# Kernel tuning notes

Hardware: AMD Instinct MI355X
Metric: run time of the kernel (lower is better)

Reference implementation:

```python
import jax, jax.numpy as jnp
import numpy as np

E = 1024   # embedding_dim
H = 16     # heads
W = 1024   # lag / seq length
B = 4      # batch
D = E // H # head dim


def setup_inputs() -> dict:
    key = jax.random.key(0)
    ks = jax.random.split(key, 5)
    scale = E ** -0.5
    return {
        "x":   jax.random.normal(ks[0], (3, B, E, W), dtype=jnp.float32),
        "L_Q": jax.random.normal(ks[1], (E, E), dtype=jnp.float32) * scale,
        "L_K": jax.random.normal(ks[2], (E, E), dtype=jnp.float32) * scale,
        "L_V": jax.random.normal(ks[3], (E, E), dtype=jnp.float32) * scale,
        "M":   jax.random.normal(ks[4], (E, E), dtype=jnp.float32) * (1.0 / (2 * E)) ** 0.5,
        "b":   jnp.zeros((E, 1), dtype=jnp.float32),
    }


def reference(x, L_Q, L_K, L_V, M, b):
    # x: [3, B, E, W] channels-first; x[0]=K input, x[1]=Q input, x[2]=V input
    K = jnp.einsum('ef,bfw->bew', L_K, x[0])
    Q = jnp.einsum('ef,bfw->bew', L_Q, x[1])
    V = jnp.einsum('ef,bfw->bew', L_V, x[2])
    # reshape to [B, H, D, W]
    Kv = K.reshape(B, H, D, W)
    Qv = Q.reshape(B, H, D, W)
    Vv = V.reshape(B, H, D, W)
    # scores[b,h,q,k] = Q_v^T @ K_v
    scores = jnp.einsum('bhdq,bhdk->bhqk', Qv, Kv)
    # causal mask: -inf for q > k (strictly lower triangle), added BEFORE softmax
    q_idx = jnp.arange(W)[:, None]
    k_idx = jnp.arange(W)[None, :]
    mask = jnp.where(q_idx > k_idx, -jnp.inf, 0.0).astype(scores.dtype)
    scores = scores + mask
    # NON-STANDARD: softmax over the QUERY axis (dim=-2), then scale
    attn = jax.nn.softmax(scores, axis=-2) / (E ** 0.5)
    # V_v @ scores: [B,H,D,W] @ [B,H,W,W] -> [B,H,D,W]
    out = jnp.einsum('bhdq,bhqk->bhdk', Vv, attn).reshape(B, E, W)
    # dense: M @ out + b (dropout identity at inference)
    return jnp.einsum('oe,bew->bow', M, out) + b
```

## Files before the change

### kernel.cpp

```cpp
#include <hip/hip_runtime.h>
#include <stdint.h>
#include <math.h>

#define E_DIM 1024
#define W_DIM 1024
#define EW 1048576L

typedef _Float16 h16;
typedef __attribute__((ext_vector_type(8))) _Float16 h8;
typedef __attribute__((ext_vector_type(4))) float f4;

__device__ __forceinline__ void async_copy16(h16* lds, const h16* g) {
    __builtin_amdgcn_global_load_lds(
        (const __attribute__((address_space(1))) void*)g,
        (__attribute__((address_space(3))) void*)lds, 16, 0, 0);
}

__global__ __launch_bounds__(256) void cvt_w(
    const float* __restrict__ a, const float* __restrict__ b,
    const float* __restrict__ c, const float* __restrict__ d,
    h16* __restrict__ out)
{
    const float* srcs[4] = {a, b, c, d};
    const int z = blockIdx.y;
    const int i = blockIdx.x * 256 + threadIdx.x;
    if (i < 262144) {
        float4 v = reinterpret_cast<const float4*>(srcs[z])[i];
        union { h16 h[4]; uint2 u; } o;
        o.h[0] = (h16)v.x; o.h[1] = (h16)v.y; o.h[2] = (h16)v.z; o.h[3] = (h16)v.w;
        reinterpret_cast<uint2*>(out + z * EW)[i] = o.u;
    }
}

__global__ __launch_bounds__(256) void cvt_t(
    const float* __restrict__ x, h16* __restrict__ xt)
{
    __shared__ float Ts[64][65];
    const long sb = blockIdx.z;
    const float* src = x + sb * EW;
    h16* dst = xt + sb * EW;
    const int e0 = blockIdx.y * 64, w0 = blockIdx.x * 64;
    const int r = threadIdx.x >> 4, c4 = (threadIdx.x & 15) * 4;

    #pragma unroll
    for (int p = 0; p < 4; ++p) {
        float4 v = *reinterpret_cast<const float4*>(src + (long)(e0 + r + p * 16) * W_DIM + w0 + c4);
        Ts[c4 + 0][r + p * 16] = v.x;
        Ts[c4 + 1][r + p * 16] = v.y;
        Ts[c4 + 2][r + p * 16] = v.z;
        Ts[c4 + 3][r + p * 16] = v.w;
    }
    __syncthreads();
    #pragma unroll
    for (int p = 0; p < 4; ++p) {
        int wr = r + p * 16;
        union { h16 h[4]; uint2 u; } o;
        o.h[0] = (h16)Ts[wr][c4 + 0];
        o.h[1] = (h16)Ts[wr][c4 + 1];
        o.h[2] = (h16)Ts[wr][c4 + 2];
        o.h[3] = (h16)Ts[wr][c4 + 3];
        *reinterpret_cast<uint2*>(dst + (long)(w0 + wr) * E_DIM + e0 + c4) = o.u;
    }
}

__global__ __launch_bounds__(256) void gemm_proj3(
    const h16* __restrict__ xh, const h16* __restrict__ Wts,
    h16* __restrict__ KQV)
{
    __shared__ h16 As[128 * 32];
    __shared__ h16 Bs[128 * 32];

    const int t = threadIdx.x;
    const int wave = t >> 6, lane = t & 63;
    const int quad = lane >> 4, l16 = lane & 15;
    const int m0 = blockIdx.y * 128, n0 = blockIdx.x * 128;
    const int wm = (wave >> 1) * 64, wn = (wave & 1) * 64;

    const int proj = blockIdx.z >> 2, bz = blockIdx.z & 3;
    const h16 *A, *Bt; h16* C;
    if (proj == 0)      { A = xh + bz * EW;       Bt = Wts;          C = KQV + bz * EW; }
    else if (proj == 1) { A = xh + (4 + bz) * EW; Bt = Wts + EW;     C = KQV + (4 + bz) * EW; }
    else                { A = Wts + 2 * EW;       Bt = xh + (8 + bz) * EW; C = KQV + (8 + bz) * EW; }

    const int sr = t >> 2;
    const int sg = (t & 3) * 8;

    f4 acc[4][4] = {};

    for (int k0 = 0; k0 < 1024; k0 += 32) {
        __syncthreads();
        async_copy16(As + sr * 32 + sg,        A  + (long)(m0 + sr) * E_DIM + k0 + sg);
        async_copy16(As + (sr + 64) * 32 + sg, A  + (long)(m0 + sr + 64) * E_DIM + k0 + sg);
        async_copy16(Bs + sr * 32 + sg,        Bt + (long)(n0 + sr) * E_DIM + k0 + sg);
        async_copy16(Bs + (sr + 64) * 32 + sg, Bt + (long)(n0 + sr + 64) * E_DIM + k0 + sg);
        __syncthreads();

        h8 av[4], bv[4];
        #pragma unroll
        for (int i = 0; i < 4; ++i) {
            av[i] = *reinterpret_cast<const h8*>(As + (wm + i * 16 + l16) * 32 + quad * 8);
            bv[i] = *reinterpret_cast<const h8*>(Bs + (wn + i * 16 + l16) * 32 + quad * 8);
        }
        #pragma unroll
        for (int mt = 0; mt < 4; ++mt)
            #pragma unroll
            for (int nt = 0; nt < 4; ++nt)
                acc[mt][nt] = __builtin_amdgcn_mfma_f32_16x16x32_f16(av[mt], bv[nt], acc[mt][nt], 0, 0, 0);
    }

    #pragma unroll
    for (int mt = 0; mt < 4; ++mt)
        #pragma unroll
        for (int i = 0; i < 4; ++i) {
            int m = m0 + wm + mt * 16 + quad * 4 + i;
            #pragma unroll
            for (int nt = 0; nt < 4; ++nt)
                C[(long)m * W_DIM + n0 + wn + nt * 16 + l16] = (h16)acc[mt][nt][i];
        }
}

__global__ __launch_bounds__(256) void gemm_out(
    const h16* __restrict__ A, const h16* __restrict__ Bt, long sBz,
    float* __restrict__ C, long sCz, const float* __restrict__ bias)
{
    __shared__ h16 As[128 * 40];
    __shared__ h16 Bs[128 * 40];

    const int t = threadIdx.x;
    const int wave = t >> 6, lane = t & 63;
    const int quad = lane >> 4, l16 = lane & 15;
    const int m0 = blockIdx.y * 128, n0 = blockIdx.x * 128;
    const int wm = (wave >> 1) * 64, wn = (wave & 1) * 64;
    Bt += blockIdx.z * sBz;

    const int sr = t >> 2;
    const int sg = (t & 3) * 8;

    f4 acc[4][4] = {};

    uint4 a0 = *reinterpret_cast<const uint4*>(A  + (long)(m0 + sr) * E_DIM + sg);
    uint4 a1 = *reinterpret_cast<const uint4*>(A  + (long)(m0 + sr + 64) * E_DIM + sg);
    uint4 b0 = *reinterpret_cast<const uint4*>(Bt + (long)(n0 + sr) * E_DIM + sg);
    uint4 b1 = *reinterpret_cast<const uint4*>(Bt + (long)(n0 + sr + 64) * E_DIM + sg);

    for (int k0 = 0; k0 < 1024; k0 += 32) {
        __syncthreads();
        *reinterpret_cast<uint4*>(As + sr * 40 + sg)        = a0;
        *reinterpret_cast<uint4*>(As + (sr + 64) * 40 + sg) = a1;
        *reinterpret_cast<uint4*>(Bs + sr * 40 + sg)        = b0;
        *reinterpret_cast<uint4*>(Bs + (sr + 64) * 40 + sg) = b1;
        __syncthreads();

        if (k0 + 32 < 1024) {
            a0 = *reinterpret_cast<const uint4*>(A  + (long)(m0 + sr) * E_DIM + k0 + 32 + sg);
            a1 = *reinterpret_cast<const uint4*>(A  + (long)(m0 + sr + 64) * E_DIM + k0 + 32 + sg);
            b0 = *reinterpret_cast<const uint4*>(Bt + (long)(n0 + sr) * E_DIM + k0 + 32 + sg);
            b1 = *reinterpret_cast<const uint4*>(Bt + (long)(n0 + sr + 64) * E_DIM + k0 + 32 + sg);
        }

        h8 av[4], bv[4];
        #pragma unroll
        for (int i = 0; i < 4; ++i) {
            av[i] = *reinterpret_cast<const h8*>(As + (wm + i * 16 + l16) * 40 + quad * 8);
            bv[i] = *reinterpret_cast<const h8*>(Bs + (wn + i * 16 + l16) * 40 + quad * 8);
        }
        #pragma unroll
        for (int mt = 0; mt < 4; ++mt)
            #pragma unroll
            for (int nt = 0; nt < 4; ++nt)
                acc[mt][nt] = __builtin_amdgcn_mfma_f32_16x16x32_f16(av[mt], bv[nt], acc[mt][nt], 0, 0, 0);
    }

    float* Cf = C + blockIdx.z * sCz;
    #pragma unroll
    for (int mt = 0; mt < 4; ++mt)
        #pragma unroll
        for (int i = 0; i < 4; ++i) {
            int m = m0 + wm + mt * 16 + quad * 4 + i;
            float bv_ = bias ? bias[m] : 0.f;
            #pragma unroll
            for (int nt = 0; nt < 4; ++nt)
                Cf[(long)m * W_DIM + n0 + wn + nt * 16 + l16] = acc[mt][nt][i] + bv_;
        }
}

__global__ __launch_bounds__(256) void attn_mfma(
    const h16* __restrict__ Kt, const h16* __restrict__ Qt,
    const h16* __restrict__ V, h16* __restrict__ AoT)
{
    __shared__ h16 Ks[64 * 72];
    __shared__ h16 Qs[64 * 72];
    __shared__ h16 Vs[64 * 72];
    __shared__ h16 Ps[4][16 * 72];

    const int t = threadIdx.x, wave = t >> 6, lane = t & 63;
    const int quad = lane >> 4, l16 = lane & 15;
    const int b = blockIdx.y >> 4, h = blockIdx.y & 15;
    const int k0 = blockIdx.x * 64;
    const int kw = wave * 16;

    const h16* Ktb = Kt + (long)b * EW + h * 64;
    const h16* Qtb = Qt + (long)b * EW + h * 64;
    const h16* Vb  = V  + (long)b * EW + (long)(h * 64) * W_DIM;

    const int sr = t >> 2;
    const int sg = (t & 3) * 8;

    uint4 ka = *reinterpret_cast<const uint4*>(Ktb + (long)(k0 + sr) * E_DIM + sg);
    uint4 kb = *reinterpret_cast<const uint4*>(Ktb + (long)(k0 + sr) * E_DIM + sg + 32);
    uint4 qa = *reinterpret_cast<const uint4*>(Qtb + (long)sr * E_DIM + sg);
    uint4 qb = *reinterpret_cast<const uint4*>(Qtb + (long)sr * E_DIM + sg + 32);
    uint4 va = *reinterpret_cast<const uint4*>(Vb + (long)sr * W_DIM + sg);
    uint4 vb = *reinterpret_cast<const uint4*>(Vb + (long)sr * W_DIM + sg + 32);

    float mrow[4], lrow[4];
    #pragma unroll
    for (int i = 0; i < 4; ++i) { mrow[i] = -1e30f; lrow[i] = 0.f; }
    f4 O[4] = {};

    for (int q0 = 0; q0 <= k0; q0 += 64) {
        __syncthreads();
        if (q0 == 0) {
            *reinterpret_cast<uint4*>(Ks + sr * 72 + sg)      = ka;
            *reinterpret_cast<uint4*>(Ks + sr * 72 + sg + 32) = kb;
        }
        *reinterpret_cast<uint4*>(Qs + sr * 72 + sg)      = qa;
        *reinterpret_cast<uint4*>(Qs + sr * 72 + sg + 32) = qb;
        *reinterpret_cast<uint4*>(Vs + sr * 72 + sg)      = va;
        *reinterpret_cast<uint4*>(Vs + sr * 72 + sg + 32) = vb;
        __syncthreads();

        if (q0 + 64 <= k0) {
            qa = *reinterpret_cast<const uint4*>(Qtb + (long)(q0 + 64 + sr) * E_DIM + sg);
            qb = *reinterpret_cast<const uint4*>(Qtb + (long)(q0 + 64 + sr) * E_DIM + sg + 32);
            va = *reinterpret_cast<const uint4*>(Vb + (long)sr * W_DIM + q0 + 64 + sg);
            vb = *reinterpret_cast<const uint4*>(Vb + (long)sr * W_DIM + q0 + 64 + sg + 32);
        }

        f4 S[4] = {};
        #pragma unroll
        for (int c = 0; c < 2; ++c) {
            h8 av = *reinterpret_cast<const h8*>(Ks + (kw + l16) * 72 + c * 32 + quad * 8);
            #pragma unroll
            for (int nt = 0; nt < 4; ++nt) {
                h8 bv = *reinterpret_cast<const h8*>(Qs + (nt * 16 + l16) * 72 + c * 32 + quad * 8);
                S[nt] = __builtin_amdgcn_mfma_f32_16x16x32_f16(av, bv, S[nt], 0, 0, 0);
            }
        }

        if (q0 == k0) {
            #pragma unroll
            for (int nt = 0; nt < 4; ++nt)
                #pragma unroll
                for (int i = 0; i < 4; ++i)
                    if (q0 + nt * 16 + l16 > k0 + kw + quad * 4 + i) S[nt][i] = -1e30f;
        }

        float al[4];
        #pragma unroll
        for (int i = 0; i < 4; ++i) {
            float mx = fmaxf(fmaxf(S[0][i], S[1][i]), fmaxf(S[2][i], S[3][i]));
            mx = fmaxf(mx, __shfl_xor(mx, 1));
            mx = fmaxf(mx, __shfl_xor(mx, 2));
            mx = fmaxf(mx, __shfl_xor(mx, 4));
            mx = fmaxf(mx, __shfl_xor(mx, 8));
            float nm = fmaxf(mrow[i], mx);
            al[i] = __expf(mrow[i] - nm);
            mrow[i] = nm;
        }
        #pragma unroll
        for (int nt = 0; nt < 4; ++nt)
            #pragma unroll
            for (int i = 0; i < 4; ++i)
                S[nt][i] = __expf(S[nt][i] - mrow[i]);
        #pragma unroll
        for (int i = 0; i < 4; ++i) {
            float sm = S[0][i] + S[1][i] + S[2][i] + S[3][i];
            sm += __shfl_xor(sm, 1);
            sm += __shfl_xor(sm, 2);
            sm += __shfl_xor(sm, 4);
            sm += __shfl_xor(sm, 8);
            lrow[i] = lrow[i] * al[i] + sm;
            #pragma unroll
            for (int dt = 0; dt < 4; ++dt) O[dt][i] *= al[i];
        }

        #pragma unroll
        for (int nt = 0; nt < 4; ++nt)
            #pragma unroll
            for (int i = 0; i < 4; ++i)
                Ps[wave][(quad * 4 + i) * 72 + nt * 16 + l16] = (h16)S[nt][i];
        asm volatile("" ::: "memory");

        #pragma unroll
        for (int c = 0; c < 2; ++c) {
            h8 pa = *reinterpret_cast<const h8*>(&Ps[wave][l16 * 72 + c * 32 + quad * 8]);
            #pragma unroll
            for (int dt = 0; dt < 4; ++dt) {
                h8 vv = *reinterpret_cast<const h8*>(Vs + (dt * 16 + l16) * 72 + c * 32 + quad * 8);
                O[dt] = __builtin_amdgcn_mfma_f32_16x16x32_f16(pa, vv, O[dt], 0, 0, 0);
            }
        }
    }

    #pragma unroll
    for (int dt = 0; dt < 4; ++dt)
        #pragma unroll
        for (int i = 0; i < 4; ++i)
            AoT[(long)b * EW + (long)(k0 + kw + quad * 4 + i) * E_DIM + h * 64 + dt * 16 + l16] =
                (h16)(O[dt][i] / lrow[i] * 0.03125f);
}

extern "C" void kernel_launch(void* const* d_in, const int* in_sizes, int n_in,
                              void* d_out, int out_size, void* d_ws, size_t ws_size,
                              hipStream_t stream)
{
    const float* x  = (const float*)d_in[0];
    const float* LQ = (const float*)d_in[1];
    const float* LK = (const float*)d_in[2];
    const float* LV = (const float*)d_in[3];
    const float* Mw = (const float*)d_in[4];
    const float* bb = (const float*)d_in[5];
    float* out = (float*)d_out;
    h16* ws = (h16*)d_ws;

    h16* xh  = ws;
    h16* LKh = ws + 12 * EW;
    h16* Mh  = ws + 15 * EW;
    h16* Kp  = ws + 16 * EW;
    h16* Qp  = ws + 20 * EW;
    h16* Vp  = ws + 24 * EW;
    h16* Ao  = ws + 28 * EW;

    cvt_w<<<dim3(1024, 4), 256, 0, stream>>>(LK, LQ, LV, Mw, LKh);
    cvt_t<<<dim3(16, 16, 12), 256, 0, stream>>>(x, xh);

    dim3 blk(256);
    gemm_proj3<<<dim3(8, 8, 12), blk, 0, stream>>>(xh, LKh, Kp);

    attn_mfma<<<dim3(16, 64), blk, 0, stream>>>(Kp, Qp, Vp, Ao);

    gemm_out<<<dim3(8, 8, 4), blk, 0, stream>>>(Mh, Ao, EW, out, EW, bb);
}
```

Measured before the change: 226.8 us.

## Fuse conversion kernels, async double-buffer attention and output GEMM, reorder tiles

Merges the weight conversion and input transpose into one prep launch. The attention kernel now keeps K fragments in registers, double-buffers Q/V tiles in XOR-swizzled LDS through async global-to-LDS copies, and launches the heaviest causal tiles first. The row-sum shuffle reduction is replaced by an MFMA against a ones vector. The output GEMM uses 64x128 tiles with async double-buffered LDS and folds the batch into the N dimension, adding more blocks at the cost of fewer accumulators per wave.

```diff
diff --git a/kernel.cpp b/kernel.cpp
--- a/kernel.cpp
+++ b/kernel.cpp
@@ -16,50 +16,51 @@
         (__attribute__((address_space(3))) void*)lds, 16, 0, 0);
 }
 
-__global__ __launch_bounds__(256) void cvt_w(
-    const float* __restrict__ a, const float* __restrict__ b,
-    const float* __restrict__ c, const float* __restrict__ d,
-    h16* __restrict__ out)
-{
-    const float* srcs[4] = {a, b, c, d};
-    const int z = blockIdx.y;
-    const int i = blockIdx.x * 256 + threadIdx.x;
-    if (i < 262144) {
-        float4 v = reinterpret_cast<const float4*>(srcs[z])[i];
-        union { h16 h[4]; uint2 u; } o;
-        o.h[0] = (h16)v.x; o.h[1] = (h16)v.y; o.h[2] = (h16)v.z; o.h[3] = (h16)v.w;
-        reinterpret_cast<uint2*>(out + z * EW)[i] = o.u;
-    }
-}
-
-__global__ __launch_bounds__(256) void cvt_t(
-    const float* __restrict__ x, h16* __restrict__ xt)
+__global__ __launch_bounds__(256) void prep(
+    const float* __restrict__ x, const float* __restrict__ LK,
+    const float* __restrict__ LQ, const float* __restrict__ LV,
+    const float* __restrict__ Mw, h16* __restrict__ xt, h16* __restrict__ wh)
 {
     __shared__ float Ts[64][65];
-    const long sb = blockIdx.z;
-    const float* src = x + sb * EW;
-    h16* dst = xt + sb * EW;
-    const int e0 = blockIdx.y * 64, w0 = blockIdx.x * 64;
-    const int r = threadIdx.x >> 4, c4 = (threadIdx.x & 15) * 4;
-
-    #pragma unroll
-    for (int p = 0; p < 4; ++p) {
-        float4 v = *reinterpret_cast<const float4*>(src + (long)(e0 + r + p * 16) * W_DIM + w0 + c4);
-        Ts[c4 + 0][r + p * 16] = v.x;
-        Ts[c4 + 1][r + p * 16] = v.y;
-        Ts[c4 + 2][r + p * 16] = v.z;
-        Ts[c4 + 3][r + p * 16] = v.w;
-    }
-    __syncthreads();
-    #pragma unroll
-    for (int p = 0; p < 4; ++p) {
-        int wr = r + p * 16;
-        union { h16 h[4]; uint2 u; } o;
-        o.h[0] = (h16)Ts[wr][c4 + 0];
-        o.h[1] = (h16)Ts[wr][c4 + 1];
-        o.h[2] = (h16)Ts[wr][c4 + 2];
-        o.h[3] = (h16)Ts[wr][c4 + 3];
-        *reinterpret_cast<uint2*>(dst + (long)(w0 + wr) * E_DIM + e0 + c4) = o.u;
+    const int z = blockIdx.z;
+    const int t = threadIdx.x;
+    if (z < 12) {
+        const float* src = x + (long)z * EW;
+        h16* dst = xt + (long)z * EW;
+        const int e0 = blockIdx.y * 64, w0 = blockIdx.x * 64;
+        const int r = t >> 4, c4 = (t & 15) * 4;
+        #pragma unroll
+        for (int p = 0; p < 4; ++p) {
+            float4 v = *reinterpret_cast<const float4*>(src + (long)(e0 + r + p * 16) * W_DIM + w0 + c4);
+            Ts[c4 + 0][r + p * 16] = v.x;
+            Ts[c4 + 1][r + p * 16] = v.y;
+            Ts[c4 + 2][r + p * 16] = v.z;
+            Ts[c4 + 3][r + p * 16] = v.w;
+        }
+        __syncthreads();
+        #pragma unroll
+        for (int p = 0; p < 4; ++p) {
+            int wr = r + p * 16;
+            union { h16 h[4]; uint2 u; } o;
+            o.h[0] = (h16)Ts[wr][c4 + 0];
+            o.h[1] = (h16)Ts[wr][c4 + 1];
+            o.h[2] = (h16)Ts[wr][c4 + 2];
+            o.h[3] = (h16)Ts[wr][c4 + 3];
+            *reinterpret_cast<uint2*>(dst + (long)(w0 + wr) * E_DIM + e0 + c4) = o.u;
+        }
+    } else {
+        const float* srcs[4] = {LK, LQ, LV, Mw};
+        const float* s = srcs[z - 12];
+        h16* o = wh + (long)(z - 12) * EW;
+        long base = ((long)(blockIdx.y * 16 + blockIdx.x)) * 1024 + t;
+        #pragma unroll
+        for (int k = 0; k < 4; ++k) {
+            long i = base + k * 256;
+            float4 v = reinterpret_cast<const float4*>(s)[i];
+            union { h16 h[4]; uint2 u; } u;
+            u.h[0] = (h16)v.x; u.h[1] = (h16)v.y; u.h[2] = (h16)v.z; u.h[3] = (h16)v.w;
+            reinterpret_cast<uint2*>(o)[i] = u.u;
+        }
     }
 }
 
@@ -120,67 +121,69 @@
 }
 
 __global__ __launch_bounds__(256) void gemm_out(
-    const h16* __restrict__ A, const h16* __restrict__ Bt, long sBz,
-    float* __restrict__ C, long sCz, const float* __restrict__ bias)
-{
-    __shared__ h16 As[128 * 40];
-    __shared__ h16 Bs[128 * 40];
+    const h16* __restrict__ A, const h16* __restrict__ Bt,
+    float* __restrict__ C, const float* __restrict__ bias)
+{
+    __shared__ h16 As[2][64 * 32];
+    __shared__ h16 Bs[2][128 * 32];
 
     const int t = threadIdx.x;
     const int wave = t >> 6, lane = t & 63;
     const int quad = lane >> 4, l16 = lane & 15;
-    const int m0 = blockIdx.y * 128, n0 = blockIdx.x * 128;
-    const int wm = (wave >> 1) * 64, wn = (wave & 1) * 64;
-    Bt += blockIdx.z * sBz;
-
-    const int sr = t >> 2;
-    const int sg = (t & 3) * 8;
-
-    f4 acc[4][4] = {};
-
-    uint4 a0 = *reinterpret_cast<const uint4*>(A  + (long)(m0 + sr) * E_DIM + sg);
-    uint4 a1 = *reinterpret_cast<const uint4*>(A  + (long)(m0 + sr + 64) * E_DIM + sg);
-    uint4 b0 = *reinterpret_cast<const uint4*>(Bt + (long)(n0 + sr) * E_DIM + sg);
-    uint4 b1 = *reinterpret_cast<const uint4*>(Bt + (long)(n0 + sr + 64) * E_DIM + sg);
-
-    for (int k0 = 0; k0 < 1024; k0 += 32) {
-        __syncthreads();
-        *reinterpret_cast<uint4*>(As + sr * 40 + sg)        = a0;
-        *reinterpret_cast<uint4*>(As + (sr + 64) * 40 + sg) = a1;
-        *reinterpret_cast<uint4*>(Bs + sr * 40 + sg)        = b0;
-        *reinterpret_cast<uint4*>(Bs + (sr + 64) * 40 + sg) = b1;
-        __syncthreads();
-
-        if (k0 + 32 < 1024) {
-            a0 = *reinterpret_cast<const uint4*>(A  + (long)(m0 + sr) * E_DIM + k0 + 32 + sg);
-            a1 = *reinterpret_cast<const uint4*>(A  + (long)(m0 + sr + 64) * E_DIM + k0 + 32 + sg);
-            b0 = *reinterpret_cast<const uint4*>(Bt + (long)(n0 + sr) * E_DIM + k0 + 32 + sg);
-            b1 = *reinterpret_cast<const uint4*>(Bt + (long)(n0 + sr + 64) * E_DIM + k0 + 32 + sg);
-        }
-
-        h8 av[4], bv[4];
-        #pragma unroll
-        for (int i = 0; i < 4; ++i) {
-            av[i] = *reinterpret_cast<const h8*>(As + (wm + i * 16 + l16) * 40 + quad * 8);
-            bv[i] = *reinterpret_cast<const h8*>(Bs + (wn + i * 16 + l16) * 40 + quad * 8);
-        }
-        #pragma unroll
-        for (int mt = 0; mt < 4; ++mt)
+    const int m0 = blockIdx.y * 64, n0 = blockIdx.x * 128;
+    const int wm = (wave >> 1) * 32, wn = (wave & 1) * 64;
+
+    f4 acc[2][4] = {};
+
+    const int ga_r = t >> 2, ga_c = (t & 3) * 8;
+
+    {
+        async_copy16(&As[0][t * 8], A + (long)(m0 + ga_r) * E_DIM + ga_c);
+        #pragma unroll
+        for (int j = 0; j < 2; ++j) {
+            int g = j * 256 + t;
+            async_copy16(&Bs[0][g * 8], Bt + (long)(n0 + (g >> 2)) * E_DIM + (g & 3) * 8);
+        }
+    }
+
+    for (int it = 0; it < 32; ++it) {
+        __syncthreads();
+        if (it + 1 < 32) {
+            int nb = (it + 1) & 1, k0 = (it + 1) * 32;
+            async_copy16(&As[nb][t * 8], A + (long)(m0 + ga_r) * E_DIM + k0 + ga_c);
+            #pragma unroll
+            for (int j = 0; j < 2; ++j) {
+                int g = j * 256 + t;
+                async_copy16(&Bs[nb][g * 8], Bt + (long)(n0 + (g >> 2)) * E_DIM + k0 + (g & 3) * 8);
+            }
+        }
+        const h16* as = As[it & 1];
+        const h16* bs = Bs[it & 1];
+        h8 av[2], bv[4];
+        #pragma unroll
+        for (int mt = 0; mt < 2; ++mt)
+            av[mt] = *reinterpret_cast<const h8*>(as + (wm + mt * 16 + l16) * 32 + quad * 8);
+        #pragma unroll
+        for (int nt = 0; nt < 4; ++nt)
+            bv[nt] = *reinterpret_cast<const h8*>(bs + (wn + nt * 16 + l16) * 32 + quad * 8);
+        #pragma unroll
+        for (int mt = 0; mt < 2; ++mt)
             #pragma unroll
             for (int nt = 0; nt < 4; ++nt)
                 acc[mt][nt] = __builtin_amdgcn_mfma_f32_16x16x32_f16(av[mt], bv[nt], acc[mt][nt], 0, 0, 0);
     }
 
-    float* Cf = C + blockIdx.z * sCz;
-    #pragma unroll
-    for (int mt = 0; mt < 4; ++mt)
+    #pragma unroll
+    for (int mt = 0; mt < 2; ++mt)
         #pragma unroll
         for (int i = 0; i < 4; ++i) {
             int m = m0 + wm + mt * 16 + quad * 4 + i;
             float bv_ = bias ? bias[m] : 0.f;
             #pragma unroll
-            for (int nt = 0; nt < 4; ++nt)
-                Cf[(long)m * W_DIM + n0 + wn + nt * 16 + l16] = acc[mt][nt][i] + bv_;
+            for (int nt = 0; nt < 4; ++nt) {
+                int n = n0 + wn + nt * 16 + l16;
+                C[(long)(n >> 10) * EW + (long)m * W_DIM + (n & 1023)] = acc[mt][nt][i] + bv_;
+            }
         }
 }
 
@@ -188,67 +191,69 @@
     const h16* __restrict__ Kt, const h16* __restrict__ Qt,
     const h16* __restrict__ V, h16* __restrict__ AoT)
 {
-    __shared__ h16 Ks[64 * 72];
-    __shared__ h16 Qs[64 * 72];
-    __shared__ h16 Vs[64 * 72];
+    __shared__ h16 Qs[2][64 * 64];
+    __shared__ h16 Vs[2][64 * 64];
     __shared__ h16 Ps[4][16 * 72];
 
     const int t = threadIdx.x, wave = t >> 6, lane = t & 63;
     const int quad = lane >> 4, l16 = lane & 15;
     const int b = blockIdx.y >> 4, h = blockIdx.y & 15;
-    const int k0 = blockIdx.x * 64;
+    const int kt = 15 - blockIdx.x;
+    const int k0 = kt * 64;
     const int kw = wave * 16;
 
     const h16* Ktb = Kt + (long)b * EW + h * 64;
     const h16* Qtb = Qt + (long)b * EW + h * 64;
     const h16* Vb  = V  + (long)b * EW + (long)(h * 64) * W_DIM;
 
-    const int sr = t >> 2;
-    const int sg = (t & 3) * 8;
-
-    uint4 ka = *reinterpret_cast<const uint4*>(Ktb + (long)(k0 + sr) * E_DIM + sg);
-    uint4 kb = *reinterpret_cast<const uint4*>(Ktb + (long)(k0 + sr) * E_DIM + sg + 32);
-    uint4 qa = *reinterpret_cast<const uint4*>(Qtb + (long)sr * E_DIM + sg);
-    uint4 qb = *reinterpret_cast<const uint4*>(Qtb + (long)sr * E_DIM + sg + 32);
-    uint4 va = *reinterpret_cast<const uint4*>(Vb + (long)sr * W_DIM + sg);
-    uint4 vb = *reinterpret_cast<const uint4*>(Vb + (long)sr * W_DIM + sg + 32);
-
-    float mrow[4], lrow[4];
-    #pragma unroll
-    for (int i = 0; i < 4; ++i) { mrow[i] = -1e30f; lrow[i] = 0.f; }
+    h8 av0 = *reinterpret_cast<const h8*>(Ktb + (long)(k0 + kw + l16) * E_DIM + quad * 8);
+    h8 av1 = *reinterpret_cast<const h8*>(Ktb + (long)(k0 + kw + l16) * E_DIM + 32 + quad * 8);
+
+    const int swz0 = ((quad) ^ (l16 & 7)) * 8;
+    const int swz1 = ((4 + quad) ^ (l16 & 7)) * 8;
+
+    float mrow[4], al[4];
+    #pragma unroll
+    for (int i = 0; i < 4; ++i) mrow[i] = -1e30f;
     f4 O[4] = {};
-
-    for (int q0 = 0; q0 <= k0; q0 += 64) {
-        __syncthreads();
-        if (q0 == 0) {
-            *reinterpret_cast<uint4*>(Ks + sr * 72 + sg)      = ka;
-            *reinterpret_cast<uint4*>(Ks + sr * 72 + sg + 32) = kb;
-        }
-        *reinterpret_cast<uint4*>(Qs + sr * 72 + sg)      = qa;
-        *reinterpret_cast<uint4*>(Qs + sr * 72 + sg + 32) = qb;
-        *reinterpret_cast<uint4*>(Vs + sr * 72 + sg)      = va;
-        *reinterpret_cast<uint4*>(Vs + sr * 72 + sg + 32) = vb;
-        __syncthreads();
-
-        if (q0 + 64 <= k0) {
-            qa = *reinterpret_cast<const uint4*>(Qtb + (long)(q0 + 64 + sr) * E_DIM + sg);
-            qb = *reinterpret_cast<const uint4*>(Qtb + (long)(q0 + 64 + sr) * E_DIM + sg + 32);
-            va = *reinterpret_cast<const uint4*>(Vb + (long)sr * W_DIM + q0 + 64 + sg);
-            vb = *reinterpret_cast<const uint4*>(Vb + (long)sr * W_DIM + q0 + 64 + sg + 32);
-        }
+    f4 Lacc = {};
+    h8 ones;
+    #pragma unroll
+    for (int j = 0; j < 8; ++j) ones[j] = (h16)1.0f;
+
+    #pragma unroll
+    for (int j = 0; j < 2; ++j) {
+        int g = j * 256 + t, row = g >> 3, cg = (g & 7) ^ (row & 7);
+        async_copy16(&Qs[0][g * 8], Qtb + (long)row * E_DIM + cg * 8);
+        async_copy16(&Vs[0][g * 8], Vb + (long)row * W_DIM + cg * 8);
+    }
+
+    for (int it = 0; it <= kt; ++it) {
+        const int q0 = it * 64;
+        __syncthreads();
+        if (it < kt) {
+            int nb = (it + 1) & 1, q1 = q0 + 64;
+            #pragma unroll
+            for (int j = 0; j < 2; ++j) {
+                int g = j * 256 + t, row = g >> 3, cg = (g & 7) ^ (row & 7);
+                async_copy16(&Qs[nb][g * 8], Qtb + (long)(q1 + row) * E_DIM + cg * 8);
+                async_copy16(&Vs[nb][g * 8], Vb + (long)row * W_DIM + q1 + cg * 8);
+            }
+        }
+        const h16* qs = Qs[it & 1];
+        const h16* vs = Vs[it & 1];
 
         f4 S[4] = {};
         #pragma unroll
-        for (int c = 0; c < 2; ++c) {
-            h8 av = *reinterpret_cast<const h8*>(Ks + (kw + l16) * 72 + c * 32 + quad * 8);
-            #pragma unroll
-            for (int nt = 0; nt < 4; ++nt) {
-                h8 bv = *reinterpret_cast<const h8*>(Qs + (nt * 16 + l16) * 72 + c * 32 + quad * 8);
-                S[nt] = __builtin_amdgcn_mfma_f32_16x16x32_f16(av, bv, S[nt], 0, 0, 0);
-            }
-        }
-
-        if (q0 == k0) {
+        for (int nt = 0; nt < 4; ++nt) {
+            int rb = (nt * 16 + l16) * 64;
+            h8 b0 = *reinterpret_cast<const h8*>(qs + rb + swz0);
+            h8 b1 = *reinterpret_cast<const h8*>(qs + rb + swz1);
+            S[nt] = __builtin_amdgcn_mfma_f32_16x16x32_f16(av0, b0, S[nt], 0, 0, 0);
+            S[nt] = __builtin_amdgcn_mfma_f32_16x16x32_f16(av1, b1, S[nt], 0, 0, 0);
+        }
+
+        if (it == kt) {
             #pragma unroll
             for (int nt = 0; nt < 4; ++nt)
                 #pragma unroll
@@ -256,7 +261,6 @@
                     if (q0 + nt * 16 + l16 > k0 + kw + quad * 4 + i) S[nt][i] = -1e30f;
         }
 
-        float al[4];
         #pragma unroll
         for (int i = 0; i < 4; ++i) {
             float mx = fmaxf(fmaxf(S[0][i], S[1][i]), fmaxf(S[2][i], S[3][i]));
@@ -275,12 +279,7 @@
                 S[nt][i] = __expf(S[nt][i] - mrow[i]);
         #pragma unroll
         for (int i = 0; i < 4; ++i) {
-            float sm = S[0][i] + S[1][i] + S[2][i] + S[3][i];
-            sm += __shfl_xor(sm, 1);
-            sm += __shfl_xor(sm, 2);
-            sm += __shfl_xor(sm, 4);
-            sm += __shfl_xor(sm, 8);
-            lrow[i] = lrow[i] * al[i] + sm;
+            Lacc[i] *= al[i];
             #pragma unroll
             for (int dt = 0; dt < 4; ++dt) O[dt][i] *= al[i];
         }
@@ -295,9 +294,11 @@
         #pragma unroll
         for (int c = 0; c < 2; ++c) {
             h8 pa = *reinterpret_cast<const h8*>(&Ps[wave][l16 * 72 + c * 32 + quad * 8]);
+            Lacc = __builtin_amdgcn_mfma_f32_16x16x32_f16(pa, ones, Lacc, 0, 0, 0);
+            int sw = c ? swz1 : swz0;
             #pragma unroll
             for (int dt = 0; dt < 4; ++dt) {
-                h8 vv = *reinterpret_cast<const h8*>(Vs + (dt * 16 + l16) * 72 + c * 32 + quad * 8);
+                h8 vv = *reinterpret_cast<const h8*>(vs + (dt * 16 + l16) * 64 + sw);
                 O[dt] = __builtin_amdgcn_mfma_f32_16x16x32_f16(pa, vv, O[dt], 0, 0, 0);
             }
         }
@@ -308,7 +309,7 @@
         #pragma unroll
         for (int i = 0; i < 4; ++i)
             AoT[(long)b * EW + (long)(k0 + kw + quad * 4 + i) * E_DIM + h * 64 + dt * 16 + l16] =
-                (h16)(O[dt][i] / lrow[i] * 0.03125f);
+                (h16)(O[dt][i] / Lacc[i] * 0.03125f);
 }
 
 extern "C" void kernel_launch(void* const* d_in, const int* in_sizes, int n_in,
@@ -332,13 +333,9 @@
     h16* Vp  = ws + 24 * EW;
     h16* Ao  = ws + 28 * EW;
 
-    cvt_w<<<dim3(1024, 4), 256, 0, stream>>>(LK, LQ, LV, Mw, LKh);
-    cvt_t<<<dim3(16, 16, 12), 256, 0, stream>>>(x, xh);
-
     dim3 blk(256);
+    prep<<<dim3(16, 16, 16), blk, 0, stream>>>(x, LK, LQ, LV, Mw, xh, LKh);
     gemm_proj3<<<dim3(8, 8, 12), blk, 0, stream>>>(xh, LKh, Kp);
-
     attn_mfma<<<dim3(16, 64), blk, 0, stream>>>(Kp, Qp, Vp, Ao);
-
-    gemm_out<<<dim3(8, 8, 4), blk, 0, stream>>>(Mh, Ao, EW, out, EW, bb);
-}
+    gemm_out<<<dim3(32, 16), blk, 0, stream>>>(Mh, Ao, out, bb);
+}
```

Result: no change. 222.6 us (-1.9%).
